# Kernel optimization log

Measured on AMD Instinct MI355X. Metric: run time of the kernel, lower is better.

The kernel has to match this reference:

```python
import jax, jax.numpy as jnp
import numpy as np

MIN_NORM = 1e-15
BALL_EPS = 0.004  # torch.float32 entry of BALL_EPS
SCALING = float(np.tanh(1.0 / 2.0))  # tanh(tau/2), tau=1.0
N_GRAPHS = 512
BN_EPS = 1e-5


def _cmin(v):
    return jnp.maximum(v, MIN_NORM)


def project(x):
    norm = _cmin(jnp.linalg.norm(x, axis=-1, keepdims=True))
    maxnorm = 1.0 - BALL_EPS
    return jnp.where(norm > maxnorm, x / norm * maxnorm, x)


def isometric_transform(x, a):
    r2 = jnp.sum(a * a, axis=-1, keepdims=True) - 1.0
    u = x - a
    return r2 / _cmin(jnp.sum(u * u, axis=-1, keepdims=True)) * u + a


def reflect_at_zero(x, mu):
    a = mu / _cmin(jnp.sum(mu * mu, axis=-1, keepdims=True))
    return isometric_transform(x, a)


def reflect_through_zero(p, q, x):
    p_ = p / _cmin(jnp.linalg.norm(p, axis=-1, keepdims=True))
    q_ = q / _cmin(jnp.linalg.norm(q, axis=-1, keepdims=True))
    r = q_ - p_
    m = jnp.sum(r * x, axis=-1, keepdims=True) / jnp.sum(r * r, axis=-1, keepdims=True)
    return x - 2.0 * r * m


def logmap0(y):
    yn = _cmin(jnp.linalg.norm(y, axis=-1, keepdims=True))
    return y / yn * jnp.arctanh(jnp.clip(yn, -1.0 + 1e-15, 1.0 - 1e-15))


def unique_rows(m):
    # Emulates torch.unique(dim=0, return_inverse=True) for all-distinct rows
    # (true w.p. 1 for continuous activations): lexicographic sort, col 0 primary.
    n = m.shape[0]
    perm = jnp.lexsort(m.T[::-1])
    inv = jnp.zeros(n, jnp.int32).at[perm].set(jnp.arange(n, dtype=jnp.int32))
    return m[perm], inv


def _forward(x, edge_index, batch, W0, b0, convW1, convb1, gamma, beta, convW2,
             convb2, fc1W, fc1b, fc2W, fc2b, fc3W, fc3b):
    n = x.shape[0]
    d = W0.shape[1]
    x = jax.nn.relu(x @ W0 + b0)
    xs = [x]
    z = [jnp.zeros((1, d), x.dtype)]
    inv = [jnp.zeros(n, jnp.int32)]
    u, iv = unique_rows(jax.lax.stop_gradient(x))  # no_grad in original
    z.append(SCALING * project(u))
    inv.append(iv)
    src, dst = edge_index[0], edge_index[1]
    n_layers = convW1.shape[0]
    p_vec = jnp.zeros((d,), x.dtype).at[-1].set(1.0)
    for i in range(n_layers):
        # GINConv (eps=0): MLP(x + sum_{j->i} x_j)
        agg = jax.ops.segment_sum(x[src], dst, num_segments=n)
        h = x + agg
        h = jax.nn.relu(h @ convW1[i] + convb1[i])
        mu = jnp.mean(h, axis=0)
        var = jnp.var(h, axis=0)  # biased, as BatchNorm1d training mode
        h = gamma[i] * (h - mu) / jnp.sqrt(var + BN_EPS) + beta[i]
        x = jax.nn.relu(h @ convW2[i] + convb2[i])
        x = x.at[:, -1].set(0.0)  # x @ diag zeroes last column
        xs.append(x)
        u_full, iv = unique_rows(jax.lax.stop_gradient(jnp.concatenate(xs, axis=1)))
        cnt = jax.ops.segment_sum(jnp.ones(n, jnp.int32), iv, num_segments=n)
        u = u_full[:, -d:]
        z_children = SCALING * project(u)
        t1 = jax.ops.segment_sum(inv[i + 1], iv, num_segments=n) // cnt
        z_current = z[i + 1][t1]
        t2 = jax.ops.segment_sum(inv[i], iv, num_segments=n) // cnt
        z_parent = z[i][t2]
        z_parent = reflect_at_zero(z_parent, z_current)
        z_children = reflect_through_zero(z_parent, p_vec, z_children)
        z_all = reflect_at_zero(z_children, z_current)
        inv.append(iv)
        z.append(z_all)
    xh = logmap0(z[-1])[inv[-1]]
    out = jax.ops.segment_sum(xh, batch, num_segments=N_GRAPHS)
    out = jax.nn.relu(out @ fc1W + fc1b)
    out = jax.nn.relu(out @ fc2W + fc2b)
    out = out @ fc3W + fc3b
    return jax.nn.log_softmax(out, axis=1)


def setup_inputs() -> dict:
    N, E, D_IN, D, L, C = 50000, 800000, 128, 64, 3, 10
    key = jax.random.key(0)
    ks = jax.random.split(key, 12)
    s = 0.05
    return {
        "x": jax.random.normal(ks[0], (N, D_IN), jnp.float32),
        "edge_index": jax.random.randint(ks[1], (2, E), 0, N),
        "batch": jnp.sort(jax.random.randint(ks[2], (N,), 0, 512)),
        "W0": jax.random.normal(ks[3], (D_IN, D), jnp.float32) * s,
        "b0": jnp.zeros((D,), jnp.float32),
        "convW1": jax.random.normal(ks[4], (L, D, D), jnp.float32) * s,
        "convb1": jnp.zeros((L, D), jnp.float32),
        "gamma": jnp.ones((L, D), jnp.float32),
        "beta": jnp.zeros((L, D), jnp.float32),
        "convW2": jax.random.normal(ks[5], (L, D, D), jnp.float32) * s,
        "convb2": jnp.zeros((L, D), jnp.float32),
        "fc1W": jax.random.normal(ks[6], (D, 128), jnp.float32) * s,
        "fc1b": jnp.zeros((128,), jnp.float32),
        "fc2W": jax.random.normal(ks[7], (128, 64), jnp.float32) * s,
        "fc2b": jnp.zeros((64,), jnp.float32),
        "fc3W": jax.random.normal(ks[8], (64, C), jnp.float32) * s,
        "fc3b": jnp.zeros((C,), jnp.float32),
    }


def reference(x, edge_index, batch, W0, b0, convW1, convb1, gamma, beta, convW2,
              convb2, fc1W, fc1b, fc2W, fc2b, fc3W, fc3b):
    return _forward(x, edge_index, batch, W0, b0, convW1, convb1, gamma, beta,
                    convW2, convb2, fc1W, fc1b, fc2W, fc2b, fc3W, fc3b)
```

## Files before the change

### kernel.cpp

```cpp
#include <hip/hip_runtime.h>
#include <hip/hip_fp16.h>
#include <math.h>

#define SCALING_F 0.46211715726000974f
#define MAXNORM_F 0.996f
#define MINNORM_F 1e-15f
#define BN_EPS_F  1e-5f

typedef _Float16 v8h __attribute__((ext_vector_type(8)));
typedef float    v4f __attribute__((ext_vector_type(4)));

__device__ __forceinline__ float rsum16(float v) {
  v += __shfl_xor(v, 1, 64);
  v += __shfl_xor(v, 2, 64);
  v += __shfl_xor(v, 4, 64);
  v += __shfl_xor(v, 8, 64);
  return v;
}

__device__ __forceinline__ void rsum16x6(float& a, float& b, float& c,
                                         float& d, float& e, float& f) {
#pragma unroll
  for (int o = 1; o <= 8; o <<= 1) {
    a += __shfl_xor(a, o, 64);
    b += __shfl_xor(b, o, 64);
    c += __shfl_xor(c, o, 64);
    d += __shfl_xor(d, o, 64);
    e += __shfl_xor(e, o, 64);
    f += __shfl_xor(f, o, 64);
  }
}

__device__ __forceinline__ float h2f(float v) {
  return __half2float(__float2half(v));
}

__device__ __forceinline__ void acc8(float* a, uint4 u) {
  __half2 h0 = *(__half2*)&u.x;
  __half2 h1 = *(__half2*)&u.y;
  __half2 h2 = *(__half2*)&u.z;
  __half2 h3 = *(__half2*)&u.w;
  a[0] += __low2float(h0); a[1] += __high2float(h0);
  a[2] += __low2float(h1); a[3] += __high2float(h1);
  a[4] += __low2float(h2); a[5] += __high2float(h2);
  a[6] += __low2float(h3); a[7] += __high2float(h3);
}

__device__ __forceinline__ void load4f(const __half* p, float* a) {
  uint2 u = *(const uint2*)p;
  __half2 h0 = *(__half2*)&u.x;
  __half2 h1 = *(__half2*)&u.y;
  a[0] = __low2float(h0); a[1] = __high2float(h0);
  a[2] = __low2float(h1); a[3] = __high2float(h1);
}

__global__ __launch_bounds__(256) void k_wcvt(
    const float* __restrict__ W0, const float* __restrict__ cW1,
    const float* __restrict__ cW2, int L,
    __half* __restrict__ W0T, __half* __restrict__ W1T, __half* __restrict__ W2T)
{
  int id = blockIdx.x * 256 + threadIdx.x;
  if (id < 64 * 128) {
    int n = id >> 7, k = id & 127;
    W0T[id] = __float2half(W0[(size_t)k * 64 + n]);
  }
  if (id < L * 64 * 64) {
    int l = id >> 12, rem = id & 4095;
    int n = rem >> 6, k = rem & 63;
    W1T[id] = __float2half(cW1[(size_t)l * 4096 + k * 64 + n]);
    W2T[id] = __float2half(cW2[(size_t)l * 4096 + k * 64 + n]);
  }
}

__global__ __launch_bounds__(256) void k_gb(const int* __restrict__ batch,
                                            int N, int G, int* __restrict__ gstart)
{
  int r = blockIdx.x * 256 + threadIdx.x;
  if (r >= N) return;
  int b = batch[r];
  int prev = (r == 0) ? -1 : batch[r - 1];
  for (int g = prev + 1; g <= b; ++g) gstart[g] = r;
  if (r == N - 1)
    for (int g = b + 1; g <= G; ++g) gstart[g] = N;
}

__global__ __launch_bounds__(256) void k_mm0(
    const float* __restrict__ A, const __half* __restrict__ BT,
    const float* __restrict__ bias, __half* __restrict__ X, int M)
{
  const int tid  = threadIdx.x;
  const int w    = tid >> 6;
  const int lane = tid & 63;
  const int q    = lane >> 4;
  const int i    = lane & 15;
  const int rblk = blockIdx.x * 64;
  const int arow = rblk + w * 16 + i;

  v4f acc[4];
#pragma unroll
  for (int t = 0; t < 4; ++t) acc[t] = (v4f){0.f, 0.f, 0.f, 0.f};

#pragma unroll
  for (int hh = 0; hh < 4; ++hh) {
    v8h af = (v8h){0, 0, 0, 0, 0, 0, 0, 0};
    if (arow < M) {
      const float* p = &A[(size_t)arow * 128 + hh * 32 + q * 8];
      float4 fa = *(const float4*)p;
      float4 fb = *(const float4*)(p + 4);
      af[0] = (_Float16)fa.x; af[1] = (_Float16)fa.y;
      af[2] = (_Float16)fa.z; af[3] = (_Float16)fa.w;
      af[4] = (_Float16)fb.x; af[5] = (_Float16)fb.y;
      af[6] = (_Float16)fb.z; af[7] = (_Float16)fb.w;
    }
#pragma unroll
    for (int t = 0; t < 4; ++t) {
      v8h bf = *(const v8h*)&BT[(size_t)(t * 16 + i) * 128 + hh * 32 + q * 8];
      acc[t] = __builtin_amdgcn_mfma_f32_16x16x32_f16(af, bf, acc[t], 0, 0, 0);
    }
  }

#pragma unroll
  for (int j = 0; j < 4; ++j) {
    int row = rblk + w * 16 + 4 * q + j;
    if (row >= M) continue;
#pragma unroll
    for (int t = 0; t < 4; ++t)
      X[(size_t)row * 64 + i + 16 * t] =
          __float2half(fmaxf(acc[t][j] + bias[i + 16 * t], 0.f));
  }
}

__global__ __launch_bounds__(256, 6) void k_layer1(
    const __half* __restrict__ x, const int* __restrict__ rowptr,
    const unsigned short* __restrict__ csr, const __half* __restrict__ BT,
    const float* __restrict__ bias, __half* __restrict__ h,
    float* __restrict__ gstat, int M)
{
  __shared__ __half AsH[64][80];
  __shared__ float st[2048];
  const int tid  = threadIdx.x;
  const int w    = tid >> 6;
  const int lane = tid & 63;
  const int q    = lane >> 4;
  const int i    = lane & 15;
  const int g8   = lane >> 3;
  const int i8   = lane & 7;
  const int rblk = blockIdx.x * 64;

  for (int pr = 0; pr < 8; ++pr) {
    int lr0 = w * 16 + 2 * pr;
    int lr1 = lr0 + 1;
    int r0 = rblk + lr0, r1 = rblk + lr1;
    bool v0 = (r0 < M), v1 = (r1 < M);
    float a0[8] = {0.f,0.f,0.f,0.f,0.f,0.f,0.f,0.f};
    float a1[8] = {0.f,0.f,0.f,0.f,0.f,0.f,0.f,0.f};
    int c0 = 0, e0 = 0, c1 = 0, e1 = 0;
    if (v0) { c0 = rowptr[r0]; e0 = rowptr[r0 + 1]; }
    if (v1) { c1 = rowptr[r1]; e1 = rowptr[r1 + 1]; }
    if (v0 && g8 == 0) acc8(a0, *(const uint4*)&x[(size_t)r0 * 64 + 8 * i8]);
    if (v1 && g8 == 0) acc8(a1, *(const uint4*)&x[(size_t)r1 * 64 + 8 * i8]);

    int n16 = (e0 - c0) >> 4;
    int m16 = (e1 - c1) >> 4;
    int cnt = (n16 < m16) ? n16 : m16;
    for (int it = 0; it < cnt; ++it) {
      int n0a = csr[c0 + g8];
      int n0b = csr[c0 + 8 + g8];
      int n1a = csr[c1 + g8];
      int n1b = csr[c1 + 8 + g8];
      uint4 u0a = *(const uint4*)&x[(size_t)n0a * 64 + 8 * i8];
      uint4 u0b = *(const uint4*)&x[(size_t)n0b * 64 + 8 * i8];
      uint4 u1a = *(const uint4*)&x[(size_t)n1a * 64 + 8 * i8];
      uint4 u1b = *(const uint4*)&x[(size_t)n1b * 64 + 8 * i8];
      acc8(a0, u0a);
      acc8(a0, u0b);
      acc8(a1, u1a);
      acc8(a1, u1b);
      c0 += 16;
      c1 += 16;
    }
    while (c0 + 8 <= e0 || c1 + 8 <= e1) {
      bool d0 = (c0 + 8 <= e0);
      bool d1 = (c1 + 8 <= e1);
      int n0 = 0, n1 = 0;
      if (d0) n0 = csr[c0 + g8];
      if (d1) n1 = csr[c1 + g8];
      uint4 u0, u1;
      if (d0) u0 = *(const uint4*)&x[(size_t)n0 * 64 + 8 * i8];
      if (d1) u1 = *(const uint4*)&x[(size_t)n1 * 64 + 8 * i8];
      if (d0) { acc8(a0, u0); c0 += 8; }
      if (d1) { acc8(a1, u1); c1 += 8; }
    }
    {
      int rem0 = e0 - c0;
      int rem1 = e1 - c1;
      int n0 = 0, n1 = 0;
      if (g8 < rem0) n0 = csr[c0 + g8];
      if (g8 < rem1) n1 = csr[c1 + g8];
      uint4 u0, u1;
      if (g8 < rem0) u0 = *(const uint4*)&x[(size_t)n0 * 64 + 8 * i8];
      if (g8 < rem1) u1 = *(const uint4*)&x[(size_t)n1 * 64 + 8 * i8];
      if (g8 < rem0) acc8(a0, u0);
      if (g8 < rem1) acc8(a1, u1);
    }
#pragma unroll
    for (int k = 0; k < 8; ++k) {
      a0[k] += __shfl_xor(a0[k], 8, 64);
      a1[k] += __shfl_xor(a1[k], 8, 64);
      a0[k] += __shfl_xor(a0[k], 16, 64);
      a1[k] += __shfl_xor(a1[k], 16, 64);
      a0[k] += __shfl_xor(a0[k], 32, 64);
      a1[k] += __shfl_xor(a1[k], 32, 64);
    }
    if (g8 == 0) {
      __half hv0[8], hv1[8];
#pragma unroll
      for (int k = 0; k < 8; ++k) { hv0[k] = __float2half(a0[k]); hv1[k] = __float2half(a1[k]); }
      *(uint4*)&AsH[lr0][8 * i8] = *(uint4*)hv0;
      *(uint4*)&AsH[lr1][8 * i8] = *(uint4*)hv1;
    }
  }
  __syncthreads();

  v4f acc[4];
#pragma unroll
  for (int t = 0; t < 4; ++t) acc[t] = (v4f){0.f, 0.f, 0.f, 0.f};
#pragma unroll
  for (int hh = 0; hh < 2; ++hh) {
    v8h af = *(const v8h*)&AsH[w * 16 + i][hh * 32 + q * 8];
#pragma unroll
    for (int t = 0; t < 4; ++t) {
      v8h bf = *(const v8h*)&BT[(size_t)(t * 16 + i) * 64 + hh * 32 + q * 8];
      acc[t] = __builtin_amdgcn_mfma_f32_16x16x32_f16(af, bf, acc[t], 0, 0, 0);
    }
  }

  float s[4] = {0.f, 0.f, 0.f, 0.f}, qq[4] = {0.f, 0.f, 0.f, 0.f};
#pragma unroll
  for (int j = 0; j < 4; ++j) {
    int row = rblk + w * 16 + 4 * q + j;
    if (row >= M) continue;
#pragma unroll
    for (int t = 0; t < 4; ++t) {
      float v = h2f(fmaxf(acc[t][j] + bias[i + 16 * t], 0.f));
      h[(size_t)row * 64 + i + 16 * t] = __float2half(v);
      s[t] += v;
      qq[t] += v * v;
    }
  }
  {
    int g = w * 4 + q;
#pragma unroll
    for (int t = 0; t < 4; ++t) {
      st[g * 64 + i + 16 * t]        = s[t];
      st[1024 + g * 64 + i + 16 * t] = qq[t];
    }
    __syncthreads();
    if (tid < 64) {
      float a = 0.f, b = 0.f;
#pragma unroll
      for (int g2 = 0; g2 < 16; ++g2) {
        a += st[g2 * 64 + tid];
        b += st[1024 + g2 * 64 + tid];
      }
      atomicAdd(&gstat[tid], a);
      atomicAdd(&gstat[64 + tid], b);
    }
  }
}

__global__ __launch_bounds__(256) void k_layer2(
    const __half* __restrict__ A, const __half* __restrict__ BT,
    const float* __restrict__ bias,
    const float* __restrict__ gstat, const float* __restrict__ gamma,
    const float* __restrict__ beta,
    __half* __restrict__ Xout, int M)
{
  __shared__ float scl_s[64], shf_s[64];
  const int tid  = threadIdx.x;
  const int w    = tid >> 6;
  const int lane = tid & 63;
  const int q    = lane >> 4;
  const int i    = lane & 15;
  const int rblk = blockIdx.x * 64;
  const int arow = rblk + w * 16 + i;

  if (tid < 64) {
    float mu  = gstat[tid] / (float)M;
    float var = gstat[64 + tid] / (float)M - mu * mu;
    float sv  = gamma[tid] / sqrtf(var + BN_EPS_F);
    scl_s[tid] = sv;
    shf_s[tid] = beta[tid] - mu * sv;
  }
  __syncthreads();

  v4f acc[4];
#pragma unroll
  for (int t = 0; t < 4; ++t) acc[t] = (v4f){0.f, 0.f, 0.f, 0.f};
#pragma unroll
  for (int hh = 0; hh < 2; ++hh) {
    const int k0 = hh * 32 + q * 8;
    v8h af = (v8h){0, 0, 0, 0, 0, 0, 0, 0};
    {
      float hv[8] = {0,0,0,0,0,0,0,0};
      if (arow < M) {
        uint4 u = *(const uint4*)&A[(size_t)arow * 64 + k0];
        __half2 h0 = *(__half2*)&u.x;
        __half2 h1 = *(__half2*)&u.y;
        __half2 h2 = *(__half2*)&u.z;
        __half2 h3 = *(__half2*)&u.w;
        hv[0] = __low2float(h0); hv[1] = __high2float(h0);
        hv[2] = __low2float(h1); hv[3] = __high2float(h1);
        hv[4] = __low2float(h2); hv[5] = __high2float(h2);
        hv[6] = __low2float(h3); hv[7] = __high2float(h3);
      }
#pragma unroll
      for (int k = 0; k < 8; ++k)
        af[k] = (_Float16)fmaf(hv[k], scl_s[k0 + k], shf_s[k0 + k]);
    }
#pragma unroll
    for (int t = 0; t < 4; ++t) {
      v8h bf = *(const v8h*)&BT[(size_t)(t * 16 + i) * 64 + k0];
      acc[t] = __builtin_amdgcn_mfma_f32_16x16x32_f16(af, bf, acc[t], 0, 0, 0);
    }
  }

#pragma unroll
  for (int j = 0; j < 4; ++j) {
    int row = rblk + w * 16 + 4 * q + j;
    if (row >= M) continue;
#pragma unroll
    for (int t = 0; t < 4; ++t) {
      float v = fmaxf(acc[t][j] + bias[i + 16 * t], 0.f);
      if (i == 15 && t == 3) v = 0.f;
      Xout[(size_t)row * 64 + i + 16 * t] = __float2half(v);
    }
  }
}

__global__ __launch_bounds__(256) void k_zchain(
    const __half* __restrict__ X0, const __half* __restrict__ X1,
    const __half* __restrict__ X2, const __half* __restrict__ X3,
    __half* __restrict__ Xh, int M)
{
  const int tid = threadIdx.x;
  const int i   = tid & 15;
  const int row = blockIdx.x * 16 + (tid >> 4);
  const bool valid = (row < M);

  float x0[4] = {0,0,0,0}, x1[4] = {0,0,0,0}, x2[4] = {0,0,0,0}, x3[4] = {0,0,0,0};
  if (valid) {
    load4f(&X0[(size_t)row * 64 + 4 * i], x0);
    load4f(&X1[(size_t)row * 64 + 4 * i], x1);
    load4f(&X2[(size_t)row * 64 + 4 * i], x2);
    load4f(&X3[(size_t)row * 64 + 4 * i], x3);
  }

  float zc[4], zp[4] = {0.f, 0.f, 0.f, 0.f};
  {
    float sx = rsum16(x0[0]*x0[0] + x0[1]*x0[1] + x0[2]*x0[2] + x0[3]*x0[3]);
    float norm = fmaxf(sqrtf(sx), MINNORM_F);
    float s = ((norm > MAXNORM_F) ? (MAXNORM_F / norm) : 1.0f) * SCALING_F;
#pragma unroll
    for (int e = 0; e < 4; ++e) zc[e] = x0[e] * s;
  }

  const float* Xi[3] = {x1, x2, x3};
#pragma unroll
  for (int li = 0; li < 3; ++li) {
    const float* xv = Xi[li];

    float p1 = xv[0]*xv[0] + xv[1]*xv[1] + xv[2]*xv[2] + xv[3]*xv[3];
    float p2 = zc[0]*zc[0]+zc[1]*zc[1]+zc[2]*zc[2]+zc[3]*zc[3];
    float p3 = zp[0]*zp[0]+zp[1]*zp[1]+zp[2]*zp[2]+zp[3]*zp[3];
    float p4 = zp[0]*zc[0]+zp[1]*zc[1]+zp[2]*zc[2]+zp[3]*zc[3];
    float p5 = zp[0]*xv[0]+zp[1]*xv[1]+zp[2]*xv[2]+zp[3]*xv[3];
    float p6 = zc[0]*xv[0]+zc[1]*xv[1]+zc[2]*xv[2]+zc[3]*xv[3];
    rsum16x6(p1, p2, p3, p4, p5, p6);
    float zc63 = __shfl(zc[3], 15, 16);
    float zp63 = __shfl(zp[3], 15, 16);

    float nzc2 = fmaxf(p2, MINNORM_F);
    float icz  = 1.0f / nzc2;
    float na2  = p2 * icz * icz;
    float r2   = na2 - 1.0f;
    float a63  = zc63 * icz;

    float sxn = fmaxf(sqrtf(p1), MINNORM_F);
    float sc  = ((sxn > MAXNORM_F) ? (MAXNORM_F / sxn) : 1.0f) * SCALING_F;
    float Sch2   = sc * sc * p1;
    float Szp_a  = p4 * icz;
    float Sa_ch  = sc * p6 * icz;
    float Szp_ch = sc * p5;
    float Su_a   = Szp_a - na2;
    float Su2    = p3 - 2.0f * Szp_a + na2;
    float nu2    = fmaxf(Su2, MINNORM_F);
    float t1     = r2 / nu2;
    float Szp22  = fmaxf(t1*t1*Su2 + 2.0f*t1*Su_a + na2, 0.0f);
    float npn    = fmaxf(sqrtf(Szp22), MINNORM_F);
    float ipn    = 1.0f / npn;
    float zp2_63 = t1 * (zp63 - a63) + a63;
    float Szp2ch = t1 * (Szp_ch - Sa_ch) + Sa_ch;
    float rdc    = -ipn * Szp2ch;
    float rdr    = 1.0f - 2.0f*ipn*zp2_63 + ipn*ipn*Szp22;
    float m2     = 2.0f * rdc / rdr;
    float Szp2a  = t1 * Su_a + na2;
    float Srr_a  = a63 - ipn * Szp2a;
    float Sc2a   = Sa_ch - m2 * Srr_a;
    float Sc22   = Sch2 - 2.0f*m2*rdc + m2*m2*rdr;
    float Sc2ma  = Sc22 - 2.0f*Sc2a + na2;
    float nu22   = fmaxf(Sc2ma, MINNORM_F);
    float t2     = r2 / nu22;

    float zn[4];
#pragma unroll
    for (int e = 0; e < 4; ++e) {
      float ai  = zc[e] * icz;
      float zp2 = t1 * (zp[e] - ai) + ai;
      float rri = ((i == 15 && e == 3) ? 1.0f : 0.0f) - ipn * zp2;
      float c2  = sc * xv[e] - m2 * rri;
      zn[e]     = t2 * (c2 - ai) + ai;
    }
#pragma unroll
    for (int e = 0; e < 4; ++e) { zp[e] = zc[e]; zc[e] = zn[e]; }
  }

  {
    float sz = rsum16(zc[0]*zc[0] + zc[1]*zc[1] + zc[2]*zc[2] + zc[3]*zc[3]);
    float yn  = fmaxf(sqrtf(sz), MINNORM_F);
    float t   = fminf(yn, 1.0f);
    float ath = 0.5f * logf((1.0f + t) / (1.0f - t));
    float wsc = ath / yn;
    if (valid) {
      __half hv[4];
      hv[0] = __float2half(zc[0] * wsc);
      hv[1] = __float2half(zc[1] * wsc);
      hv[2] = __float2half(zc[2] * wsc);
      hv[3] = __float2half(zc[3] * wsc);
      *(uint2*)&Xh[(size_t)row * 64 + 4 * i] = *(uint2*)hv;
    }
  }
}

__global__ __launch_bounds__(256) void k_deg(const int* __restrict__ dst, int E, int* deg) {
  int i0 = (blockIdx.x * 256 + threadIdx.x) * 4;
  if (i0 + 4 <= E) {
    int4 d = *(const int4*)&dst[i0];
    atomicAdd(&deg[d.x], 1);
    atomicAdd(&deg[d.y], 1);
    atomicAdd(&deg[d.z], 1);
    atomicAdd(&deg[d.w], 1);
  } else {
    for (int i = i0; i < E; ++i) atomicAdd(&deg[dst[i]], 1);
  }
}

__global__ __launch_bounds__(256) void k_scan1(const int* __restrict__ deg, int N,
                                               int* rowptr, int* bsum) {
  __shared__ int s[256];
  int t = threadIdx.x;
  int i = blockIdx.x * 256 + t;
  int v = (i < N) ? deg[i] : 0;
  s[t] = v;
  __syncthreads();
  for (int d = 1; d < 256; d <<= 1) {
    int add = (t >= d) ? s[t - d] : 0;
    __syncthreads();
    s[t] += add;
    __syncthreads();
  }
  if (i < N) rowptr[i] = s[t] - v;
  if (t == 255) bsum[blockIdx.x] = s[255];
}

__global__ __launch_bounds__(256) void k_scan2(const int* __restrict__ bsum, int NB, int* boff) {
  __shared__ int s[256];
  int t = threadIdx.x;
  int v = (t < NB) ? bsum[t] : 0;
  s[t] = v;
  __syncthreads();
  for (int d = 1; d < 256; d <<= 1) {
    int add = (t >= d) ? s[t - d] : 0;
    __syncthreads();
    s[t] += add;
    __syncthreads();
  }
  boff[t] = s[t] - v;
}

__global__ __launch_bounds__(256) void k_scan3(int* rowptr, const int* __restrict__ boff,
                                               int* cursor, int N, int E) {
  int i = blockIdx.x * 256 + threadIdx.x;
  if (i < N) {
    int v = rowptr[i] + boff[blockIdx.x];
    rowptr[i] = v;
    cursor[i] = v;
  }
  if (i == 0) rowptr[N] = E;
}

__global__ __launch_bounds__(256) void k_fill(const int* __restrict__ src,
                                              const int* __restrict__ dst, int E,
                                              int* cursor, unsigned short* __restrict__ csr) {
  int i0 = (blockIdx.x * 256 + threadIdx.x) * 4;
  if (i0 + 4 <= E) {
    int4 d = *(const int4*)&dst[i0];
    int4 s = *(const int4*)&src[i0];
    int p0 = atomicAdd(&cursor[d.x], 1);
    int p1 = atomicAdd(&cursor[d.y], 1);
    int p2 = atomicAdd(&cursor[d.z], 1);
    int p3 = atomicAdd(&cursor[d.w], 1);
    csr[p0] = (unsigned short)s.x;
    csr[p1] = (unsigned short)s.y;
    csr[p2] = (unsigned short)s.z;
    csr[p3] = (unsigned short)s.w;
  } else {
    for (int i = i0; i < E; ++i) {
      int p = atomicAdd(&cursor[dst[i]], 1);
      csr[p] = (unsigned short)src[i];
    }
  }
}

__global__ __launch_bounds__(128) void k_mlp(const __half* __restrict__ Xh,
                                             const int* __restrict__ gstart,
                                             const float* __restrict__ fc1W, const float* __restrict__ fc1b,
                                             const float* __restrict__ fc2W, const float* __restrict__ fc2b,
                                             const float* __restrict__ fc3W, const float* __restrict__ fc3b,
                                             float* __restrict__ out) {
  __shared__ float p2s[2][64];
  __shared__ float p[64], o1[128], o2[64], lg[10], red[2];
  int g = blockIdx.x, t = threadIdx.x;
  int beg = gstart[g], end = gstart[g + 1];
  {
    int half = t >> 6, c = t & 63;
    float a = 0.f;
    int r = beg + half;
    for (; r + 6 <= end; r += 8) {
      float v0 = __half2float(Xh[(size_t)(r + 0) * 64 + c]);
      float v1 = __half2float(Xh[(size_t)(r + 2) * 64 + c]);
      float v2 = __half2float(Xh[(size_t)(r + 4) * 64 + c]);
      float v3 = __half2float(Xh[(size_t)(r + 6) * 64 + c]);
      a += (v0 + v1) + (v2 + v3);
    }
    for (; r < end; r += 2) a += __half2float(Xh[(size_t)r * 64 + c]);
    p2s[half][c] = a;
  }
  __syncthreads();
  if (t < 64) p[t] = p2s[0][t] + p2s[1][t];
  __syncthreads();
  {
    float a = fc1b[t];
    for (int k = 0; k < 64; ++k) a = fmaf(p[k], fc1W[k * 128 + t], a);
    o1[t] = fmaxf(a, 0.f);
  }
  __syncthreads();
  if (t < 64) {
    float a = fc2b[t];
    for (int k = 0; k < 128; ++k) a = fmaf(o1[k], fc2W[k * 64 + t], a);
    o2[t] = fmaxf(a, 0.f);
  }
  __syncthreads();
  if (t < 10) {
    float a = fc3b[t];
    for (int k = 0; k < 64; ++k) a = fmaf(o2[k], fc3W[k * 10 + t], a);
    lg[t] = a;
  }
  __syncthreads();
  if (t == 0) {
    float mx = lg[0];
    for (int j = 1; j < 10; ++j) mx = fmaxf(mx, lg[j]);
    float s = 0.f;
    for (int j = 0; j < 10; ++j) s += expf(lg[j] - mx);
    red[0] = mx;
    red[1] = logf(s);
  }
  __syncthreads();
  if (t < 10) out[(size_t)g * 10 + t] = lg[t] - red[0] - red[1];
}

extern "C" void kernel_launch(void* const* d_in, const int* in_sizes, int n_in,
                              void* d_out, int out_size, void* d_ws, size_t ws_size,
                              hipStream_t stream) {
  const float* x_in  = (const float*)d_in[0];
  const int*   ei    = (const int*)d_in[1];
  const int*   batch = (const int*)d_in[2];
  const float* W0    = (const float*)d_in[3];
  const float* b0    = (const float*)d_in[4];
  const float* cW1   = (const float*)d_in[5];
  const float* cb1   = (const float*)d_in[6];
  const float* gamma = (const float*)d_in[7];
  const float* beta  = (const float*)d_in[8];
  const float* cW2   = (const float*)d_in[9];
  const float* cb2   = (const float*)d_in[10];
  const float* fc1W  = (const float*)d_in[11];
  const float* fc1b  = (const float*)d_in[12];
  const float* fc2W  = (const float*)d_in[13];
  const float* fc2b  = (const float*)d_in[14];
  const float* fc3W  = (const float*)d_in[15];
  const float* fc3b  = (const float*)d_in[16];
  float* out = (float*)d_out;

  const int N = in_sizes[0] / 128;
  const int E = in_sizes[1] / 2;
  const int L = in_sizes[5] / (64 * 64);
  const int G = out_size / 10;
  const int* src = ei;
  const int* dst = ei + E;

  char* ws = (char*)d_ws;
  size_t off = 0;
  auto alloc = [&](size_t bytes) -> char* {
    char* p = ws + off;
    off += (bytes + 255) & ~(size_t)255;
    return p;
  };
  __half* X0  = (__half*)alloc((size_t)N * 64 * 2);
  __half* X1  = (__half*)alloc((size_t)N * 64 * 2);
  __half* X2  = (__half*)alloc((size_t)N * 64 * 2);
  __half* X3  = (__half*)alloc((size_t)N * 64 * 2);
  __half* Bf  = (__half*)alloc((size_t)N * 64 * 2);
  __half* Xh  = (__half*)alloc((size_t)N * 64 * 2);
  __half* W0T = (__half*)alloc((size_t)64 * 128 * 2);
  __half* W1T = (__half*)alloc((size_t)L * 64 * 64 * 2);
  __half* W2T = (__half*)alloc((size_t)L * 64 * 64 * 2);
  int*    gstart = (int*)alloc((size_t)(G + 1) * 4);
  int*   deg  = (int*)alloc((size_t)N * 4);
  float* gstatAll = (float*)alloc((size_t)3 * 128 * 4);
  char*  zero_end = ws + off;
  int*   rowptr = (int*)alloc((size_t)(N + 1) * 4);
  int*   cursor = (int*)alloc((size_t)N * 4);
  unsigned short* csr = (unsigned short*)alloc((size_t)E * 2);
  int*   bsum   = (int*)alloc(256 * 4);
  int*   boff   = (int*)alloc(256 * 4);
  __half* Xs[4] = {X0, X1, X2, X3};

  hipMemsetAsync(deg, 0, (size_t)(zero_end - (char*)deg), stream);

  const int mmGrid    = (N + 63) / 64;
  const int zcGrid    = (N + 15) / 16;
  const int edge4Grid = (E / 4 + 255) / 256 + 1;
  const int wcvtGrid  = (((L * 4096 > 8192) ? L * 4096 : 8192) + 255) / 256;

  k_wcvt<<<wcvtGrid, 256, 0, stream>>>(W0, cW1, cW2, L, W0T, W1T, W2T);
  k_gb<<<(N + 255) / 256, 256, 0, stream>>>(batch, N, G, gstart);

  k_mm0<<<mmGrid, 256, 0, stream>>>(x_in, W0T, b0, X0, N);

  k_deg<<<edge4Grid, 256, 0, stream>>>(dst, E, deg);
  const int NB = (N + 255) / 256;
  k_scan1<<<NB, 256, 0, stream>>>(deg, N, rowptr, bsum);
  k_scan2<<<1, 256, 0, stream>>>(bsum, NB, boff);
  k_scan3<<<NB, 256, 0, stream>>>(rowptr, boff, cursor, N, E);
  k_fill<<<edge4Grid, 256, 0, stream>>>(src, dst, E, cursor, csr);

  for (int i = 0; i < L; ++i) {
    float* gstat = gstatAll + (size_t)i * 128;
    k_layer1<<<mmGrid, 256, 0, stream>>>(Xs[i], rowptr, csr,
                                         W1T + (size_t)i * 4096, cb1 + i * 64,
                                         Bf, gstat, N);
    k_layer2<<<mmGrid, 256, 0, stream>>>(Bf, W2T + (size_t)i * 4096, cb2 + i * 64,
                                         gstat, gamma + i * 64, beta + i * 64,
                                         Xs[i + 1], N);
  }

  k_zchain<<<zcGrid, 256, 0, stream>>>(X0, X1, X2, X3, Xh, N);

  k_mlp<<<G, 128, 0, stream>>>(Xh, gstart, fc1W, fc1b, fc2W, fc2b, fc3W, fc3b, out);
}
```

Measured before the change: 408.8 us.

## Shrink layer1 blocks to 16 rows and spread BN stat atomics over buckets

New measurement: 360.5 us. 11.8% less time.

```diff
diff --git a/kernel.cpp b/kernel.cpp
--- a/kernel.cpp
+++ b/kernel.cpp
@@ -6,6 +6,8 @@
 #define MAXNORM_F 0.996f
 #define MINNORM_F 1e-15f
 #define BN_EPS_F  1e-5f
+
+#define NBUCKET 32
 
 typedef _Float16 v8h __attribute__((ext_vector_type(8)));
 typedef float    v4f __attribute__((ext_vector_type(4)));
@@ -134,10 +136,9 @@
     const __half* __restrict__ x, const int* __restrict__ rowptr,
     const unsigned short* __restrict__ csr, const __half* __restrict__ BT,
     const float* __restrict__ bias, __half* __restrict__ h,
-    float* __restrict__ gstat, int M)
+    float* __restrict__ gstatP, int M)
 {
-  __shared__ __half AsH[64][80];
-  __shared__ float st[2048];
+  __shared__ __half AsH[16][80];
   const int tid  = threadIdx.x;
   const int w    = tid >> 6;
   const int lane = tid & 63;
@@ -145,127 +146,123 @@
   const int i    = lane & 15;
   const int g8   = lane >> 3;
   const int i8   = lane & 7;
-  const int rblk = blockIdx.x * 64;
-
-  for (int pr = 0; pr < 8; ++pr) {
-    int lr0 = w * 16 + 2 * pr;
-    int lr1 = lr0 + 1;
-    int r0 = rblk + lr0, r1 = rblk + lr1;
-    bool v0 = (r0 < M), v1 = (r1 < M);
-    float a0[8] = {0.f,0.f,0.f,0.f,0.f,0.f,0.f,0.f};
-    float a1[8] = {0.f,0.f,0.f,0.f,0.f,0.f,0.f,0.f};
-    int c0 = 0, e0 = 0, c1 = 0, e1 = 0;
-    if (v0) { c0 = rowptr[r0]; e0 = rowptr[r0 + 1]; }
-    if (v1) { c1 = rowptr[r1]; e1 = rowptr[r1 + 1]; }
-    if (v0 && g8 == 0) acc8(a0, *(const uint4*)&x[(size_t)r0 * 64 + 8 * i8]);
-    if (v1 && g8 == 0) acc8(a1, *(const uint4*)&x[(size_t)r1 * 64 + 8 * i8]);
-
-    int n16 = (e0 - c0) >> 4;
-    int m16 = (e1 - c1) >> 4;
-    int cnt = (n16 < m16) ? n16 : m16;
-    for (int it = 0; it < cnt; ++it) {
-      int n0a = csr[c0 + g8];
-      int n0b = csr[c0 + 8 + g8];
-      int n1a = csr[c1 + g8];
-      int n1b = csr[c1 + 8 + g8];
-      uint4 u0a = *(const uint4*)&x[(size_t)n0a * 64 + 8 * i8];
-      uint4 u0b = *(const uint4*)&x[(size_t)n0b * 64 + 8 * i8];
-      uint4 u1a = *(const uint4*)&x[(size_t)n1a * 64 + 8 * i8];
-      uint4 u1b = *(const uint4*)&x[(size_t)n1b * 64 + 8 * i8];
-      acc8(a0, u0a);
-      acc8(a0, u0b);
-      acc8(a1, u1a);
-      acc8(a1, u1b);
-      c0 += 16;
-      c1 += 16;
-    }
-    while (c0 + 8 <= e0 || c1 + 8 <= e1) {
-      bool d0 = (c0 + 8 <= e0);
-      bool d1 = (c1 + 8 <= e1);
-      int n0 = 0, n1 = 0;
-      if (d0) n0 = csr[c0 + g8];
-      if (d1) n1 = csr[c1 + g8];
-      uint4 u0, u1;
-      if (d0) u0 = *(const uint4*)&x[(size_t)n0 * 64 + 8 * i8];
-      if (d1) u1 = *(const uint4*)&x[(size_t)n1 * 64 + 8 * i8];
-      if (d0) { acc8(a0, u0); c0 += 8; }
-      if (d1) { acc8(a1, u1); c1 += 8; }
-    }
-    {
-      int rem0 = e0 - c0;
-      int rem1 = e1 - c1;
-      int n0 = 0, n1 = 0;
-      if (g8 < rem0) n0 = csr[c0 + g8];
-      if (g8 < rem1) n1 = csr[c1 + g8];
-      uint4 u0, u1;
-      if (g8 < rem0) u0 = *(const uint4*)&x[(size_t)n0 * 64 + 8 * i8];
-      if (g8 < rem1) u1 = *(const uint4*)&x[(size_t)n1 * 64 + 8 * i8];
-      if (g8 < rem0) acc8(a0, u0);
-      if (g8 < rem1) acc8(a1, u1);
-    }
-#pragma unroll
-    for (int k = 0; k < 8; ++k) {
-      a0[k] += __shfl_xor(a0[k], 8, 64);
-      a1[k] += __shfl_xor(a1[k], 8, 64);
-      a0[k] += __shfl_xor(a0[k], 16, 64);
-      a1[k] += __shfl_xor(a1[k], 16, 64);
-      a0[k] += __shfl_xor(a0[k], 32, 64);
-      a1[k] += __shfl_xor(a1[k], 32, 64);
-    }
-    if (g8 == 0) {
-      __half hv0[8], hv1[8];
-#pragma unroll
-      for (int k = 0; k < 8; ++k) { hv0[k] = __float2half(a0[k]); hv1[k] = __float2half(a1[k]); }
-      *(uint4*)&AsH[lr0][8 * i8] = *(uint4*)hv0;
-      *(uint4*)&AsH[lr1][8 * i8] = *(uint4*)hv1;
-    }
-  }
-  __syncthreads();
-
-  v4f acc[4];
-#pragma unroll
-  for (int t = 0; t < 4; ++t) acc[t] = (v4f){0.f, 0.f, 0.f, 0.f};
+  const int rblk = blockIdx.x * 16;
+
+  const int r0 = rblk + w * 4 + 0;
+  const int r1 = rblk + w * 4 + 1;
+  const int r2 = rblk + w * 4 + 2;
+  const int r3 = rblk + w * 4 + 3;
+  const bool v0 = (r0 < M), v1 = (r1 < M), v2 = (r2 < M), v3 = (r3 < M);
+
+  float a0[8] = {0.f,0.f,0.f,0.f,0.f,0.f,0.f,0.f};
+  float a1[8] = {0.f,0.f,0.f,0.f,0.f,0.f,0.f,0.f};
+  float a2[8] = {0.f,0.f,0.f,0.f,0.f,0.f,0.f,0.f};
+  float a3[8] = {0.f,0.f,0.f,0.f,0.f,0.f,0.f,0.f};
+
+  int c0 = 0, e0 = 0, c1 = 0, e1 = 0, c2 = 0, e2 = 0, c3 = 0, e3 = 0;
+  if (v0) { c0 = rowptr[r0]; e0 = rowptr[r0 + 1]; }
+  if (v1) { c1 = rowptr[r1]; e1 = rowptr[r1 + 1]; }
+  if (v2) { c2 = rowptr[r2]; e2 = rowptr[r2 + 1]; }
+  if (v3) { c3 = rowptr[r3]; e3 = rowptr[r3 + 1]; }
+
+  if (v0 && g8 == 0) acc8(a0, *(const uint4*)&x[(size_t)r0 * 64 + 8 * i8]);
+  if (v1 && g8 == 0) acc8(a1, *(const uint4*)&x[(size_t)r1 * 64 + 8 * i8]);
+  if (v2 && g8 == 0) acc8(a2, *(const uint4*)&x[(size_t)r2 * 64 + 8 * i8]);
+  if (v3 && g8 == 0) acc8(a3, *(const uint4*)&x[(size_t)r3 * 64 + 8 * i8]);
+
+  while ((c0 + 8 <= e0) | (c1 + 8 <= e1) | (c2 + 8 <= e2) | (c3 + 8 <= e3)) {
+    const bool d0 = (c0 + 8 <= e0);
+    const bool d1 = (c1 + 8 <= e1);
+    const bool d2 = (c2 + 8 <= e2);
+    const bool d3 = (c3 + 8 <= e3);
+    int n0 = 0, n1 = 0, n2 = 0, n3 = 0;
+    if (d0) n0 = csr[c0 + g8];
+    if (d1) n1 = csr[c1 + g8];
+    if (d2) n2 = csr[c2 + g8];
+    if (d3) n3 = csr[c3 + g8];
+    uint4 u0, u1, u2, u3;
+    if (d0) u0 = *(const uint4*)&x[(size_t)n0 * 64 + 8 * i8];
+    if (d1) u1 = *(const uint4*)&x[(size_t)n1 * 64 + 8 * i8];
+    if (d2) u2 = *(const uint4*)&x[(size_t)n2 * 64 + 8 * i8];
+    if (d3) u3 = *(const uint4*)&x[(size_t)n3 * 64 + 8 * i8];
+    if (d0) { acc8(a0, u0); c0 += 8; }
+    if (d1) { acc8(a1, u1); c1 += 8; }
+    if (d2) { acc8(a2, u2); c2 += 8; }
+    if (d3) { acc8(a3, u3); c3 += 8; }
+  }
+  {
+    const int rem0 = e0 - c0;
+    const int rem1 = e1 - c1;
+    const int rem2 = e2 - c2;
+    const int rem3 = e3 - c3;
+    int n0 = 0, n1 = 0, n2 = 0, n3 = 0;
+    if (g8 < rem0) n0 = csr[c0 + g8];
+    if (g8 < rem1) n1 = csr[c1 + g8];
+    if (g8 < rem2) n2 = csr[c2 + g8];
+    if (g8 < rem3) n3 = csr[c3 + g8];
+    uint4 u0, u1, u2, u3;
+    if (g8 < rem0) u0 = *(const uint4*)&x[(size_t)n0 * 64 + 8 * i8];
+    if (g8 < rem1) u1 = *(const uint4*)&x[(size_t)n1 * 64 + 8 * i8];
+    if (g8 < rem2) u2 = *(const uint4*)&x[(size_t)n2 * 64 + 8 * i8];
+    if (g8 < rem3) u3 = *(const uint4*)&x[(size_t)n3 * 64 + 8 * i8];
+    if (g8 < rem0) acc8(a0, u0);
+    if (g8 < rem1) acc8(a1, u1);
+    if (g8 < rem2) acc8(a2, u2);
+    if (g8 < rem3) acc8(a3, u3);
+  }
+
+#pragma unroll
+  for (int k = 0; k < 8; ++k) {
+#pragma unroll
+    for (int o = 8; o <= 32; o <<= 1) {
+      a0[k] += __shfl_xor(a0[k], o, 64);
+      a1[k] += __shfl_xor(a1[k], o, 64);
+      a2[k] += __shfl_xor(a2[k], o, 64);
+      a3[k] += __shfl_xor(a3[k], o, 64);
+    }
+  }
+  if (g8 == 0) {
+    __half hv[8];
+#pragma unroll
+    for (int k = 0; k < 8; ++k) hv[k] = __float2half(a0[k]);
+    *(uint4*)&AsH[w * 4 + 0][8 * i8] = *(uint4*)hv;
+#pragma unroll
+    for (int k = 0; k < 8; ++k) hv[k] = __float2half(a1[k]);
+    *(uint4*)&AsH[w * 4 + 1][8 * i8] = *(uint4*)hv;
+#pragma unroll
+    for (int k = 0; k < 8; ++k) hv[k] = __float2half(a2[k]);
+    *(uint4*)&AsH[w * 4 + 2][8 * i8] = *(uint4*)hv;
+#pragma unroll
+    for (int k = 0; k < 8; ++k) hv[k] = __float2half(a3[k]);
+    *(uint4*)&AsH[w * 4 + 3][8 * i8] = *(uint4*)hv;
+  }
+  __syncthreads();
+
+  v4f acc = (v4f){0.f, 0.f, 0.f, 0.f};
 #pragma unroll
   for (int hh = 0; hh < 2; ++hh) {
-    v8h af = *(const v8h*)&AsH[w * 16 + i][hh * 32 + q * 8];
-#pragma unroll
-    for (int t = 0; t < 4; ++t) {
-      v8h bf = *(const v8h*)&BT[(size_t)(t * 16 + i) * 64 + hh * 32 + q * 8];
-      acc[t] = __builtin_amdgcn_mfma_f32_16x16x32_f16(af, bf, acc[t], 0, 0, 0);
-    }
-  }
-
-  float s[4] = {0.f, 0.f, 0.f, 0.f}, qq[4] = {0.f, 0.f, 0.f, 0.f};
+    v8h af = *(const v8h*)&AsH[i][hh * 32 + q * 8];
+    v8h bf = *(const v8h*)&BT[(size_t)(w * 16 + i) * 64 + hh * 32 + q * 8];
+    acc = __builtin_amdgcn_mfma_f32_16x16x32_f16(af, bf, acc, 0, 0, 0);
+  }
+
+  const int col = w * 16 + i;
+  float s = 0.f, qq = 0.f;
 #pragma unroll
   for (int j = 0; j < 4; ++j) {
-    int row = rblk + w * 16 + 4 * q + j;
+    int row = rblk + 4 * q + j;
     if (row >= M) continue;
-#pragma unroll
-    for (int t = 0; t < 4; ++t) {
-      float v = h2f(fmaxf(acc[t][j] + bias[i + 16 * t], 0.f));
-      h[(size_t)row * 64 + i + 16 * t] = __float2half(v);
-      s[t] += v;
-      qq[t] += v * v;
-    }
-  }
-  {
-    int g = w * 4 + q;
-#pragma unroll
-    for (int t = 0; t < 4; ++t) {
-      st[g * 64 + i + 16 * t]        = s[t];
-      st[1024 + g * 64 + i + 16 * t] = qq[t];
-    }
-    __syncthreads();
-    if (tid < 64) {
-      float a = 0.f, b = 0.f;
-#pragma unroll
-      for (int g2 = 0; g2 < 16; ++g2) {
-        a += st[g2 * 64 + tid];
-        b += st[1024 + g2 * 64 + tid];
-      }
-      atomicAdd(&gstat[tid], a);
-      atomicAdd(&gstat[64 + tid], b);
-    }
+    float v = h2f(fmaxf(acc[j] + bias[col], 0.f));
+    h[(size_t)row * 64 + col] = __float2half(v);
+    s += v;
+    qq += v * v;
+  }
+  s  += __shfl_xor(s, 16, 64);  qq += __shfl_xor(qq, 16, 64);
+  s  += __shfl_xor(s, 32, 64);  qq += __shfl_xor(qq, 32, 64);
+  if (q == 0) {
+    const int bkt = (blockIdx.x & (NBUCKET - 1)) * 128;
+    atomicAdd(&gstatP[bkt + col], s);
+    atomicAdd(&gstatP[bkt + 64 + col], qq);
   }
 }
 
@@ -277,6 +274,7 @@
     __half* __restrict__ Xout, int M)
 {
   __shared__ float scl_s[64], shf_s[64];
+  __shared__ float tmp[128];
   const int tid  = threadIdx.x;
   const int w    = tid >> 6;
   const int lane = tid & 63;
@@ -285,9 +283,16 @@
   const int rblk = blockIdx.x * 64;
   const int arow = rblk + w * 16 + i;
 
+  if (tid < 128) {
+    float a = 0.f;
+#pragma unroll
+    for (int b2 = 0; b2 < NBUCKET; ++b2) a += gstat[b2 * 128 + tid];
+    tmp[tid] = a;
+  }
+  __syncthreads();
   if (tid < 64) {
-    float mu  = gstat[tid] / (float)M;
-    float var = gstat[64 + tid] / (float)M - mu * mu;
+    float mu  = tmp[tid] / (float)M;
+    float var = tmp[64 + tid] / (float)M - mu * mu;
     float sv  = gamma[tid] / sqrtf(var + BN_EPS_F);
     scl_s[tid] = sv;
     shf_s[tid] = beta[tid] - mu * sv;
@@ -626,7 +631,7 @@
   __half* W2T = (__half*)alloc((size_t)L * 64 * 64 * 2);
   int*    gstart = (int*)alloc((size_t)(G + 1) * 4);
   int*   deg  = (int*)alloc((size_t)N * 4);
-  float* gstatAll = (float*)alloc((size_t)3 * 128 * 4);
+  float* gstatAll = (float*)alloc((size_t)3 * NBUCKET * 128 * 4);
   char*  zero_end = ws + off;
   int*   rowptr = (int*)alloc((size_t)(N + 1) * 4);
   int*   cursor = (int*)alloc((size_t)N * 4);
@@ -638,6 +643,7 @@
   hipMemsetAsync(deg, 0, (size_t)(zero_end - (char*)deg), stream);
 
   const int mmGrid    = (N + 63) / 64;
+  const int l1Grid    = (N + 15) / 16;
   const int zcGrid    = (N + 15) / 16;
   const int edge4Grid = (E / 4 + 255) / 256 + 1;
   const int wcvtGrid  = (((L * 4096 > 8192) ? L * 4096 : 8192) + 255) / 256;
@@ -655,8 +661,8 @@
   k_fill<<<edge4Grid, 256, 0, stream>>>(src, dst, E, cursor, csr);
 
   for (int i = 0; i < L; ++i) {
-    float* gstat = gstatAll + (size_t)i * 128;
-    k_layer1<<<mmGrid, 256, 0, stream>>>(Xs[i], rowptr, csr,
+    float* gstat = gstatAll + (size_t)i * NBUCKET * 128;
+    k_layer1<<<l1Grid, 256, 0, stream>>>(Xs[i], rowptr, csr,
                                          W1T + (size_t)i * 4096, cb1 + i * 64,
                                          Bf, gstat, N);
     k_layer2<<<mmGrid, 256, 0, stream>>>(Bf, W2T + (size_t)i * 4096, cb2 + i * 64,
```
